# Optimization experiments

Hardware: AMD Instinct MI355X
Metric: run time of the kernel (lower is better)

The kernel has to match this reference:

```python
import jax, jax.numpy as jnp
import numpy as np
from jax.ops import segment_sum, segment_max

N_NODES = 50000
N_EDGES = 800000
N_GRAPHS = 512


def setup_inputs() -> dict:
    key = jax.random.key(0)
    ks = jax.random.split(key, 12)
    s = 0.1
    x = jax.random.normal(ks[0], (N_NODES, 3), dtype=jnp.float32)
    edge_index = jax.random.randint(ks[1], (2, N_EDGES), 0, N_NODES, dtype=jnp.int64)
    batch = jnp.sort(jax.random.randint(ks[2], (N_NODES,), 0, N_GRAPHS, dtype=jnp.int64))
    # GATConv(3, 64, heads=4): W [3, 4*64], att [4,64] each
    W1 = jax.random.normal(ks[3], (3, 256), dtype=jnp.float32) * s
    att_src1 = jax.random.normal(ks[4], (4, 64), dtype=jnp.float32) * s
    att_dst1 = jax.random.normal(ks[5], (4, 64), dtype=jnp.float32) * s
    bias1 = jnp.zeros((256,), dtype=jnp.float32)
    # GATConv(256, 128, heads=1)
    W2 = jax.random.normal(ks[6], (256, 128), dtype=jnp.float32) * s
    att_src2 = jax.random.normal(ks[7], (1, 128), dtype=jnp.float32) * s
    att_dst2 = jax.random.normal(ks[8], (1, 128), dtype=jnp.float32) * s
    bias2 = jnp.zeros((128,), dtype=jnp.float32)
    # Linear(128, 2)
    fcW = jax.random.normal(ks[9], (128, 2), dtype=jnp.float32) * s
    fcb = jnp.zeros((2,), dtype=jnp.float32)
    return {"x": x, "edge_index": edge_index, "batch": batch,
            "W1": W1, "att_src1": att_src1, "att_dst1": att_dst1, "bias1": bias1,
            "W2": W2, "att_src2": att_src2, "att_dst2": att_dst2, "bias2": bias2,
            "fcW": fcW, "fcb": fcb}


def gat_conv(x, src, dst, W, att_src, att_dst, bias):
    """PyG-style GATConv (concat heads). src->dst messages, softmax over dst."""
    N = x.shape[0]
    H, C = att_src.shape
    h = (x @ W).reshape(N, H, C)                      # [N,H,C]
    a_src = jnp.einsum('nhc,hc->nh', h, att_src)      # [N,H]
    a_dst = jnp.einsum('nhc,hc->nh', h, att_dst)      # [N,H]
    e = jax.nn.leaky_relu(a_src[src] + a_dst[dst], 0.2)  # [E,H]
    # segment softmax over incoming edges of each dst node
    emax = segment_max(e, dst, num_segments=N)        # [N,H]
    ee = jnp.exp(e - emax[dst])
    denom = segment_sum(ee, dst, num_segments=N)      # [N,H]
    alpha = ee / (denom[dst] + 1e-16)                 # [E,H]
    out = segment_sum(alpha[:, :, None] * h[src], dst, num_segments=N)  # [N,H,C]
    return out.reshape(N, H * C) + bias


def reference(x, edge_index, batch, W1, att_src1, att_dst1, bias1,
              W2, att_src2, att_dst2, bias2, fcW, fcb):
    N = x.shape[0]
    loops = jnp.arange(N, dtype=edge_index.dtype)
    src = jnp.concatenate([edge_index[0], loops])     # add self-loops (PyG default)
    dst = jnp.concatenate([edge_index[1], loops])
    h = jax.nn.relu(gat_conv(x, src, dst, W1, att_src1, att_dst1, bias1))
    h = jax.nn.relu(gat_conv(h, src, dst, W2, att_src2, att_dst2, bias2))
    # global mean pool per graph
    sums = segment_sum(h, batch, num_segments=N_GRAPHS)                # [G,128]
    counts = segment_sum(jnp.ones((N, 1), h.dtype), batch, num_segments=N_GRAPHS)
    pooled = sums / jnp.maximum(counts, 1.0)
    return pooled @ fcW + fcb                          # [G,2]
```

## Files before the change

### kernel.cpp

```cpp
#include <hip/hip_runtime.h>
#include <hip/hip_bf16.h>

#define NN 50000
#define NE 800000
#define ET (NN + NE)
#define NG 512
#define NCHUNK 196
#define NROWPAD 50048
#define CAP 64

#define NBUK 782
#define BCAP 1536
#define BSTRIDE 16

#define SCAT_BLKS 831
#define A1P_BLKS 196
#define W2B_BLKS 128
#define BND_BLKS 3
#define FRONT_GRID (SCAT_BLKS + A1P_BLKS + W2B_BLKS + BND_BLKS)

typedef __attribute__((ext_vector_type(8))) short bf16x8;
typedef __attribute__((ext_vector_type(4))) float f32x4;

static __device__ __forceinline__ float lrelu(float x) { return x > 0.f ? x : 0.2f * x; }

static __device__ __forceinline__ ushort f2b(float f) {
    __hip_bfloat16 b = __float2bfloat16(f);
    return *(ushort*)&b;
}
static __device__ __forceinline__ float b2f(ushort u) {
    union { unsigned int i; float f; } v; v.i = ((unsigned int)u) << 16; return v.f;
}

__global__ __launch_bounds__(256) void k_front(
        const int* __restrict__ ei, int* __restrict__ bcnt, unsigned int* __restrict__ bstore,
        const float* __restrict__ x, const float* __restrict__ W1,
        const float* __restrict__ attS1, const float* __restrict__ attD1,
        float* __restrict__ xa1, float* __restrict__ a1d,
        const float* __restrict__ W2, ushort* __restrict__ wtb,
        const int* __restrict__ batch, int* __restrict__ bounds) {
    __shared__ float wsd[24];
    int b = blockIdx.x, tid = threadIdx.x;
    if (b < SCAT_BLKS) {
        int t = b * 256 + tid;
        int base = t * 4;
        if (base >= ET) return;
        int4 sv, dv;
        if (base < NE) {
            sv = *(const int4*)(ei + base);
            dv = *(const int4*)(ei + NE + base);
        } else {
            int ls = base - NE;
            sv.x = ls; sv.y = ls + 1; sv.z = ls + 2; sv.w = ls + 3;
            dv = sv;
        }
        int b0 = dv.x >> 6, b1 = dv.y >> 6, b2 = dv.z >> 6, b3 = dv.w >> 6;
        int p0 = atomicAdd(&bcnt[b0 * BSTRIDE], 1);
        int p1 = atomicAdd(&bcnt[b1 * BSTRIDE], 1);
        int p2 = atomicAdd(&bcnt[b2 * BSTRIDE], 1);
        int p3 = atomicAdd(&bcnt[b3 * BSTRIDE], 1);
        bstore[b0 * BCAP + p0] = ((unsigned int)sv.x << 6) | (unsigned int)(dv.x & 63);
        bstore[b1 * BCAP + p1] = ((unsigned int)sv.y << 6) | (unsigned int)(dv.y & 63);
        bstore[b2 * BCAP + p2] = ((unsigned int)sv.z << 6) | (unsigned int)(dv.z & 63);
        bstore[b3 * BCAP + p3] = ((unsigned int)sv.w << 6) | (unsigned int)(dv.w & 63);
    } else if (b < SCAT_BLKS + A1P_BLKS) {
        if (tid < 24) {
            int sel = tid / 12, r = tid % 12;
            int i = r >> 2, h = r & 3;
            const float* att = sel ? attD1 : attS1;
            float s = 0.f;
            for (int c = 0; c < 64; c++) s += W1[i * 256 + h * 64 + c] * att[h * 64 + c];
            wsd[tid] = s;
        }
        __syncthreads();
        int n = (b - SCAT_BLKS) * 256 + tid;
        if (n >= NN) return;
        float x0 = x[n * 3], x1 = x[n * 3 + 1], x2 = x[n * 3 + 2];
        float4 r0, r1, dd;
        r0.x = x0; r0.y = x1; r0.z = x2;
        r0.w = x0 * wsd[0] + x1 * wsd[4] + x2 * wsd[8];
        r1.x = x0 * wsd[1] + x1 * wsd[5] + x2 * wsd[9];
        r1.y = x0 * wsd[2] + x1 * wsd[6] + x2 * wsd[10];
        r1.z = x0 * wsd[3] + x1 * wsd[7] + x2 * wsd[11];
        r1.w = 0.f;
        dd.x = x0 * wsd[12] + x1 * wsd[16] + x2 * wsd[20];
        dd.y = x0 * wsd[13] + x1 * wsd[17] + x2 * wsd[21];
        dd.z = x0 * wsd[14] + x1 * wsd[18] + x2 * wsd[22];
        dd.w = x0 * wsd[15] + x1 * wsd[19] + x2 * wsd[23];
        *(float4*)(xa1 + n * 8) = r0;
        *(float4*)(xa1 + n * 8 + 4) = r1;
        *(float4*)(a1d + n * 4) = dd;
    } else if (b < SCAT_BLKS + A1P_BLKS + W2B_BLKS) {
        int i = (b - SCAT_BLKS - A1P_BLKS) * 256 + tid;
        int k = i >> 7, c = i & 127;
        wtb[c * 256 + k] = f2b(W2[i]);
    } else {
        int g = (b - SCAT_BLKS - A1P_BLKS - W2B_BLKS) * 256 + tid;
        if (g > NG) return;
        int lo = 0, hi = NN;
        while (lo < hi) { int mid = (lo + hi) >> 1; if (batch[mid] < g) lo = mid + 1; else hi = mid; }
        bounds[g] = lo;
    }
}

__global__ __launch_bounds__(256) void k_csr(const int* __restrict__ bcnt,
                                             const unsigned int* __restrict__ bstore,
                                             ushort* __restrict__ csr, int* __restrict__ cnt) {
    __shared__ int cur[64];
    int b = blockIdx.x, tid = threadIdx.x;
    if (tid < 64) cur[tid] = 0;
    __syncthreads();
    int nb = bcnt[b * BSTRIDE];
    const unsigned int* bp = bstore + (size_t)b * BCAP;
    for (int i = tid; i < nb; i += 256) {
        unsigned int r = bp[i];
        int dlow = r & 63;
        int src = r >> 6;
        int pos = atomicAdd(&cur[dlow], 1);
        csr[(((size_t)b << 6) + dlow) * CAP + pos] = (ushort)src;
    }
    __syncthreads();
    if (tid < 64) {
        int node = (b << 6) + tid;
        if (node < NN) cnt[node] = cur[tid];
    }
}

__global__ void k_l1_aggr2(const float* __restrict__ xa1, const float* __restrict__ a1d,
                           const int* __restrict__ cnt, const ushort* __restrict__ csr,
                           float* __restrict__ xb) {
    int n = blockIdx.x * 256 + threadIdx.x;
    if (n >= NN) return;
    float4 ad = *(const float4*)(a1d + n * 4);
    int dg = cnt[n];
    const ushort* cp = csr + n * CAP;
    float a[4][3], l[4];
#pragma unroll
    for (int h = 0; h < 4; h++) { a[h][0] = a[h][1] = a[h][2] = 0.f; l[h] = 0.f; }
    int j = 0;
    for (; j + 4 <= dg; j += 4) {
        ushort4 ss = *(const ushort4*)(cp + j);
        int s0 = ss.x, s1 = ss.y, s2 = ss.z, s3 = ss.w;
        float4 p00 = *(const float4*)(xa1 + s0 * 8), p01 = *(const float4*)(xa1 + s0 * 8 + 4);
        float4 p10 = *(const float4*)(xa1 + s1 * 8), p11 = *(const float4*)(xa1 + s1 * 8 + 4);
        float4 p20 = *(const float4*)(xa1 + s2 * 8), p21 = *(const float4*)(xa1 + s2 * 8 + 4);
        float4 p30 = *(const float4*)(xa1 + s3 * 8), p31 = *(const float4*)(xa1 + s3 * 8 + 4);
#pragma unroll
        for (int q = 0; q < 4; q++) {
            float4 ra = (q == 0) ? p00 : (q == 1) ? p10 : (q == 2) ? p20 : p30;
            float4 rb = (q == 0) ? p01 : (q == 1) ? p11 : (q == 2) ? p21 : p31;
            float e0 = __expf(lrelu(ra.w + ad.x));
            float e1 = __expf(lrelu(rb.x + ad.y));
            float e2 = __expf(lrelu(rb.y + ad.z));
            float e3 = __expf(lrelu(rb.z + ad.w));
            a[0][0] = fmaf(e0, ra.x, a[0][0]); a[0][1] = fmaf(e0, ra.y, a[0][1]); a[0][2] = fmaf(e0, ra.z, a[0][2]); l[0] += e0;
            a[1][0] = fmaf(e1, ra.x, a[1][0]); a[1][1] = fmaf(e1, ra.y, a[1][1]); a[1][2] = fmaf(e1, ra.z, a[1][2]); l[1] += e1;
            a[2][0] = fmaf(e2, ra.x, a[2][0]); a[2][1] = fmaf(e2, ra.y, a[2][1]); a[2][2] = fmaf(e2, ra.z, a[2][2]); l[2] += e2;
            a[3][0] = fmaf(e3, ra.x, a[3][0]); a[3][1] = fmaf(e3, ra.y, a[3][1]); a[3][2] = fmaf(e3, ra.z, a[3][2]); l[3] += e3;
        }
    }
    for (; j < dg; j++) {
        int s = cp[j];
        float4 ra = *(const float4*)(xa1 + s * 8);
        float4 rb = *(const float4*)(xa1 + s * 8 + 4);
        float e0 = __expf(lrelu(ra.w + ad.x));
        float e1 = __expf(lrelu(rb.x + ad.y));
        float e2 = __expf(lrelu(rb.y + ad.z));
        float e3 = __expf(lrelu(rb.z + ad.w));
        a[0][0] = fmaf(e0, ra.x, a[0][0]); a[0][1] = fmaf(e0, ra.y, a[0][1]); a[0][2] = fmaf(e0, ra.z, a[0][2]); l[0] += e0;
        a[1][0] = fmaf(e1, ra.x, a[1][0]); a[1][1] = fmaf(e1, ra.y, a[1][1]); a[1][2] = fmaf(e1, ra.z, a[1][2]); l[1] += e1;
        a[2][0] = fmaf(e2, ra.x, a[2][0]); a[2][1] = fmaf(e2, ra.y, a[2][1]); a[2][2] = fmaf(e2, ra.z, a[2][2]); l[2] += e2;
        a[3][0] = fmaf(e3, ra.x, a[3][0]); a[3][1] = fmaf(e3, ra.y, a[3][1]); a[3][2] = fmaf(e3, ra.z, a[3][2]); l[3] += e3;
    }
    float o[12];
#pragma unroll
    for (int h = 0; h < 4; h++) {
        float inv = 1.f / (l[h] + 1e-16f);
        o[h * 3 + 0] = a[h][0] * inv;
        o[h * 3 + 1] = a[h][1] * inv;
        o[h * 3 + 2] = a[h][2] * inv;
    }
    *(float4*)(xb + n * 12) = *(float4*)(o);
    *(float4*)(xb + n * 12 + 4) = *(float4*)(o + 4);
    *(float4*)(xb + n * 12 + 8) = *(float4*)(o + 8);
}

__global__ __launch_bounds__(64) void k_gemm_mfma(
        const float* __restrict__ xb, const float* __restrict__ W1g,
        const float* __restrict__ b1g, const ushort* __restrict__ wtb,
        const float* __restrict__ attS2, const float* __restrict__ attD2,
        ushort* __restrict__ h2b, float* __restrict__ a2s, float* __restrict__ a2d) {
    __shared__ float W1s[768];
    __shared__ float b1s[256];
    int lane = threadIdx.x;
    int R = blockIdx.x * 32;
    if (R >= NN) return;
    for (int q = lane; q < 768; q += 64) W1s[q] = W1g[q];
    for (int q = lane; q < 256; q += 64) b1s[q] = b1g[q];
    __syncthreads();
    int row16 = lane & 15, kg = lane >> 4;

    float xr[2][12];
#pragma unroll
    for (int t = 0; t < 2; t++) {
        int row = R + t * 16 + row16;
        if (row < NN) {
            *(float4*)(&xr[t][0]) = *(const float4*)(xb + row * 12);
            *(float4*)(&xr[t][4]) = *(const float4*)(xb + row * 12 + 4);
            *(float4*)(&xr[t][8]) = *(const float4*)(xb + row * 12 + 8);
        } else {
#pragma unroll
            for (int q = 0; q < 12; q++) xr[t][q] = 0.f;
        }
    }

    f32x4 acc[2][8];
#pragma unroll
    for (int t = 0; t < 2; t++)
#pragma unroll
        for (int ct = 0; ct < 8; ct++) acc[t][ct] = (f32x4){0.f, 0.f, 0.f, 0.f};

    const ushort* Bb = wtb + (size_t)row16 * 256 + kg * 8;
#pragma unroll
    for (int s = 0; s < 8; s++) {
        int head = s >> 1;
        int c0 = s * 32 + kg * 8;
        bf16x8 a0, a1;
#pragma unroll
        for (int jj = 0; jj < 8; jj++) {
            int c = c0 + jj;
            float w0 = W1s[c], w1 = W1s[256 + c], w2 = W1s[512 + c], bb = b1s[c];
            float v0 = fmaxf(fmaf(xr[0][head * 3], w0, fmaf(xr[0][head * 3 + 1], w1, fmaf(xr[0][head * 3 + 2], w2, bb))), 0.f);
            float v1 = fmaxf(fmaf(xr[1][head * 3], w0, fmaf(xr[1][head * 3 + 1], w1, fmaf(xr[1][head * 3 + 2], w2, bb))), 0.f);
            a0[jj] = (short)f2b(v0);
            a1[jj] = (short)f2b(v1);
        }
#pragma unroll
        for (int ct = 0; ct < 8; ct++) {
            bf16x8 bfr = *(const bf16x8*)(Bb + ct * 16 * 256 + s * 32);
            acc[0][ct] = __builtin_amdgcn_mfma_f32_16x16x32_bf16(a0, bfr, acc[0][ct], 0, 0, 0);
            acc[1][ct] = __builtin_amdgcn_mfma_f32_16x16x32_bf16(a1, bfr, acc[1][ct], 0, 0, 0);
        }
    }

    float s2v[8], d2v[8];
#pragma unroll
    for (int ct = 0; ct < 8; ct++) {
        s2v[ct] = attS2[ct * 16 + row16];
        d2v[ct] = attD2[ct * 16 + row16];
    }
#pragma unroll
    for (int tau = 0; tau < 2; tau++) {
#pragma unroll
        for (int q = 0; q < 4; q++) {
            int row = R + tau * 16 + kg * 4 + q;
            float ps = 0.f, pd = 0.f;
            if (row < NN) {
#pragma unroll
                for (int ct = 0; ct < 8; ct++) {
                    float v = acc[tau][ct][q];
                    h2b[(size_t)row * 128 + ct * 16 + row16] = f2b(v);
                    ps = fmaf(v, s2v[ct], ps);
                    pd = fmaf(v, d2v[ct], pd);
                }
            }
            for (int o = 1; o < 16; o <<= 1) {
                ps += __shfl_xor(ps, o, 64);
                pd += __shfl_xor(pd, o, 64);
            }
            if (row < NN && row16 == 0) { a2s[row] = ps; a2d[row] = pd; }
        }
    }
}

__global__ void k_l2_aggr(const ushort* __restrict__ h2u, const float* __restrict__ a2s,
                          const float* __restrict__ a2d, const int* __restrict__ cnt,
                          const ushort* __restrict__ csr, const float* __restrict__ b2,
                          float* __restrict__ out2) {
    int n = blockIdx.x, t = threadIdx.x;
    float adm = a2d[n];
    int dg = cnt[n];
    const ushort* cp = csr + n * CAP;
    float accx = 0.f, accy = 0.f, l = 0.f;
    int j = 0;
    for (; j + 8 <= dg; j += 8) {
        ushort4 sA = *(const ushort4*)(cp + j);
        ushort4 sB = *(const ushort4*)(cp + j + 4);
        int s0 = sA.x, s1 = sA.y, s2 = sA.z, s3 = sA.w;
        int s4 = sB.x, s5 = sB.y, s6 = sB.z, s7 = sB.w;
        float e0 = a2s[s0], e1 = a2s[s1], e2 = a2s[s2], e3 = a2s[s3];
        float e4 = a2s[s4], e5 = a2s[s5], e6 = a2s[s6], e7 = a2s[s7];
        ushort2 u0 = *(const ushort2*)(h2u + (size_t)s0 * 128 + t * 2);
        ushort2 u1 = *(const ushort2*)(h2u + (size_t)s1 * 128 + t * 2);
        ushort2 u2 = *(const ushort2*)(h2u + (size_t)s2 * 128 + t * 2);
        ushort2 u3 = *(const ushort2*)(h2u + (size_t)s3 * 128 + t * 2);
        ushort2 u4 = *(const ushort2*)(h2u + (size_t)s4 * 128 + t * 2);
        ushort2 u5 = *(const ushort2*)(h2u + (size_t)s5 * 128 + t * 2);
        ushort2 u6 = *(const ushort2*)(h2u + (size_t)s6 * 128 + t * 2);
        ushort2 u7 = *(const ushort2*)(h2u + (size_t)s7 * 128 + t * 2);
        float p0 = __expf(lrelu(e0 + adm)), p1 = __expf(lrelu(e1 + adm));
        float p2 = __expf(lrelu(e2 + adm)), p3 = __expf(lrelu(e3 + adm));
        float p4 = __expf(lrelu(e4 + adm)), p5 = __expf(lrelu(e5 + adm));
        float p6 = __expf(lrelu(e6 + adm)), p7 = __expf(lrelu(e7 + adm));
        accx = fmaf(p0, b2f(u0.x), fmaf(p1, b2f(u1.x), fmaf(p2, b2f(u2.x), fmaf(p3, b2f(u3.x), accx))));
        accx = fmaf(p4, b2f(u4.x), fmaf(p5, b2f(u5.x), fmaf(p6, b2f(u6.x), fmaf(p7, b2f(u7.x), accx))));
        accy = fmaf(p0, b2f(u0.y), fmaf(p1, b2f(u1.y), fmaf(p2, b2f(u2.y), fmaf(p3, b2f(u3.y), accy))));
        accy = fmaf(p4, b2f(u4.y), fmaf(p5, b2f(u5.y), fmaf(p6, b2f(u6.y), fmaf(p7, b2f(u7.y), accy))));
        l += (p0 + p1) + (p2 + p3) + (p4 + p5) + (p6 + p7);
    }
    for (; j < dg; j++) {
        int s = cp[j];
        float p = __expf(lrelu(a2s[s] + adm));
        ushort2 u = *(const ushort2*)(h2u + (size_t)s * 128 + t * 2);
        accx = fmaf(p, b2f(u.x), accx);
        accy = fmaf(p, b2f(u.y), accy);
        l += p;
    }
    float inv = 1.f / (l + 1e-16f);
    int c = t * 2;
    float2 o;
    o.x = fmaxf(accx * inv + b2[c], 0.f);
    o.y = fmaxf(accy * inv + b2[c + 1], 0.f);
    *(float2*)(out2 + n * 128 + c) = o;
}

__global__ void k_pool_fc(const float* __restrict__ out2, const int* __restrict__ bounds,
                          const float* __restrict__ fcW, const float* __restrict__ fcb,
                          float* __restrict__ out) {
    int g = blockIdx.x, t = threadIdx.x;
    int s = bounds[g], e = bounds[g + 1];
    float s0 = 0.f, s1 = 0.f, s2 = 0.f, s3 = 0.f;
    int n = s;
    for (; n + 4 <= e; n += 4) {
        s0 += out2[n * 128 + t];
        s1 += out2[(n + 1) * 128 + t];
        s2 += out2[(n + 2) * 128 + t];
        s3 += out2[(n + 3) * 128 + t];
    }
    for (; n < e; n++) s0 += out2[n * 128 + t];
    float sum = (s0 + s1) + (s2 + s3);
    float cnt = (float)(e - s);
    float pooled = sum / fmaxf(cnt, 1.f);
    float p0 = pooled * fcW[t * 2 + 0];
    float p1 = pooled * fcW[t * 2 + 1];
    for (int o = 32; o; o >>= 1) {
        p0 += __shfl_down(p0, o, 64);
        p1 += __shfl_down(p1, o, 64);
    }
    __shared__ float l0[2], l1[2];
    if ((t & 63) == 0) { l0[t >> 6] = p0; l1[t >> 6] = p1; }
    __syncthreads();
    if (t == 0) {
        out[g * 2 + 0] = l0[0] + l0[1] + fcb[0];
        out[g * 2 + 1] = l1[0] + l1[1] + fcb[1];
    }
}

extern "C" void kernel_launch(void* const* d_in, const int* in_sizes, int n_in,
                              void* d_out, int out_size, void* d_ws, size_t ws_size,
                              hipStream_t stream) {
    (void)in_sizes; (void)n_in; (void)out_size; (void)ws_size;
    const float* x     = (const float*)d_in[0];
    const int*   ei    = (const int*)d_in[1];
    const int*   batch = (const int*)d_in[2];
    const float* W1    = (const float*)d_in[3];
    const float* attS1 = (const float*)d_in[4];
    const float* attD1 = (const float*)d_in[5];
    const float* b1    = (const float*)d_in[6];
    const float* W2    = (const float*)d_in[7];
    const float* attS2 = (const float*)d_in[8];
    const float* attD2 = (const float*)d_in[9];
    const float* b2    = (const float*)d_in[10];
    const float* fcW   = (const float*)d_in[11];
    const float* fcb   = (const float*)d_in[12];
    float* out = (float*)d_out;

    char* ws = (char*)d_ws;
    size_t off = 0;
    auto alloc = [&](size_t bytes) -> char* {
        char* p = ws + off;
        off = (off + bytes + 255) & ~(size_t)255;
        return p;
    };
    float*  xa1  = (float*)alloc((size_t)NN * 8 * 4);
    float*  a1d  = (float*)alloc((size_t)NN * 4 * 4);
    float*  xb   = (float*)alloc((size_t)NN * 12 * 4);
    int*    cnt  = (int*)alloc((size_t)NN * 4);
    ushort* csr  = (ushort*)alloc((size_t)NN * CAP * 2);
    int*    bcnt = (int*)alloc((size_t)NBUK * BSTRIDE * 4);
    unsigned int* bstore = (unsigned int*)alloc((size_t)NBUK * BCAP * 4);
    ushort* wtb  = (ushort*)alloc((size_t)128 * 256 * 2);
    ushort* h2b  = (ushort*)alloc((size_t)NN * 128 * 2);
    float*  a2s  = (float*)alloc((size_t)NN * 4);
    float*  a2d  = (float*)alloc((size_t)NN * 4);
    int*    bounds = (int*)alloc((size_t)(NG + 1) * 4);
    float*  out2 = (float*)alloc((size_t)NN * 128 * 4);

    hipMemsetAsync(bcnt, 0, (size_t)NBUK * BSTRIDE * 4, stream);
    k_front<<<FRONT_GRID, 256, 0, stream>>>(ei, bcnt, bstore, x, W1, attS1, attD1,
                                            xa1, a1d, W2, wtb, batch, bounds);
    k_csr<<<NBUK, 256, 0, stream>>>(bcnt, bstore, csr, cnt);
    k_l1_aggr2<<<NCHUNK, 256, 0, stream>>>(xa1, a1d, cnt, csr, xb);
    k_gemm_mfma<<<(NROWPAD / 32), 64, 0, stream>>>(xb, W1, b1, wtb, attS2, attD2, h2b, a2s, a2d);
    k_l2_aggr<<<NN, 64, 0, stream>>>(h2b, a2s, a2d, cnt, csr, b2, out2);
    k_pool_fc<<<NG, 128, 0, stream>>>(out2, bounds, fcW, fcb, out);
}
```

Before: 154.9 us.

## Pre-bin edges in shared memory before global bucket scatter, add self-loops in CSR

Each scatter block now bins its 1024 edges by destination into shared-memory sub-buckets of 256 nodes, then reserves space in the global bucket with one atomic per bin and writes the records out contiguously. This replaces per-edge global atomics on 782 buckets with far fewer atomics on 196 larger buckets. Self-loops are no longer scattered as edges; the CSR kernel appends them directly per node. The risks are overflow of the fixed 32-slot local bins and 5120-slot global buckets, plus the shared-memory footprint of roughly 26KB per block, which may limit occupancy.

```diff
diff --git a/kernel.cpp b/kernel.cpp
--- a/kernel.cpp
+++ b/kernel.cpp
@@ -3,17 +3,17 @@
 
 #define NN 50000
 #define NE 800000
-#define ET (NN + NE)
 #define NG 512
 #define NCHUNK 196
 #define NROWPAD 50048
 #define CAP 64
 
-#define NBUK 782
-#define BCAP 1536
+#define NBUK 196
+#define BCAP 5120
 #define BSTRIDE 16
-
-#define SCAT_BLKS 831
+#define LBCAP 32
+
+#define SCAT_BLKS 782
 #define A1P_BLKS 196
 #define W2B_BLKS 128
 #define BND_BLKS 3
@@ -39,31 +39,43 @@
         float* __restrict__ xa1, float* __restrict__ a1d,
         const float* __restrict__ W2, ushort* __restrict__ wtb,
         const int* __restrict__ batch, int* __restrict__ bounds) {
-    __shared__ float wsd[24];
     int b = blockIdx.x, tid = threadIdx.x;
     if (b < SCAT_BLKS) {
+        __shared__ unsigned int lrec[NBUK * LBCAP];
+        __shared__ int lcnt[NBUK];
+        __shared__ int lbase[NBUK];
+        for (int i = tid; i < NBUK; i += 256) lcnt[i] = 0;
+        __syncthreads();
         int t = b * 256 + tid;
-        int base = t * 4;
-        if (base >= ET) return;
-        int4 sv, dv;
-        if (base < NE) {
-            sv = *(const int4*)(ei + base);
-            dv = *(const int4*)(ei + NE + base);
-        } else {
-            int ls = base - NE;
-            sv.x = ls; sv.y = ls + 1; sv.z = ls + 2; sv.w = ls + 3;
-            dv = sv;
-        }
-        int b0 = dv.x >> 6, b1 = dv.y >> 6, b2 = dv.z >> 6, b3 = dv.w >> 6;
-        int p0 = atomicAdd(&bcnt[b0 * BSTRIDE], 1);
-        int p1 = atomicAdd(&bcnt[b1 * BSTRIDE], 1);
-        int p2 = atomicAdd(&bcnt[b2 * BSTRIDE], 1);
-        int p3 = atomicAdd(&bcnt[b3 * BSTRIDE], 1);
-        bstore[b0 * BCAP + p0] = ((unsigned int)sv.x << 6) | (unsigned int)(dv.x & 63);
-        bstore[b1 * BCAP + p1] = ((unsigned int)sv.y << 6) | (unsigned int)(dv.y & 63);
-        bstore[b2 * BCAP + p2] = ((unsigned int)sv.z << 6) | (unsigned int)(dv.z & 63);
-        bstore[b3 * BCAP + p3] = ((unsigned int)sv.w << 6) | (unsigned int)(dv.w & 63);
+        int base4 = t * 4;
+        if (base4 < NE) {
+            int4 sv = *(const int4*)(ei + base4);
+            int4 dv = *(const int4*)(ei + NE + base4);
+            int d, s, bin, p;
+            d = dv.x; s = sv.x; bin = d >> 8;
+            p = atomicAdd(&lcnt[bin], 1);
+            lrec[bin * LBCAP + p] = ((unsigned int)s << 8) | (unsigned int)(d & 255);
+            d = dv.y; s = sv.y; bin = d >> 8;
+            p = atomicAdd(&lcnt[bin], 1);
+            lrec[bin * LBCAP + p] = ((unsigned int)s << 8) | (unsigned int)(d & 255);
+            d = dv.z; s = sv.z; bin = d >> 8;
+            p = atomicAdd(&lcnt[bin], 1);
+            lrec[bin * LBCAP + p] = ((unsigned int)s << 8) | (unsigned int)(d & 255);
+            d = dv.w; s = sv.w; bin = d >> 8;
+            p = atomicAdd(&lcnt[bin], 1);
+            lrec[bin * LBCAP + p] = ((unsigned int)s << 8) | (unsigned int)(d & 255);
+        }
+        __syncthreads();
+        for (int i = tid; i < NBUK; i += 256)
+            lbase[i] = lcnt[i] ? atomicAdd(&bcnt[i * BSTRIDE], lcnt[i]) : 0;
+        __syncthreads();
+        for (int i = tid; i < NBUK * LBCAP; i += 256) {
+            int bin = i >> 5, pos = i & (LBCAP - 1);
+            if (pos < lcnt[bin])
+                bstore[(size_t)bin * BCAP + lbase[bin] + pos] = lrec[i];
+        }
     } else if (b < SCAT_BLKS + A1P_BLKS) {
+        __shared__ float wsd[24];
         if (tid < 24) {
             int sel = tid / 12, r = tid % 12;
             int i = r >> 2, h = r & 3;
@@ -106,23 +118,25 @@
 __global__ __launch_bounds__(256) void k_csr(const int* __restrict__ bcnt,
                                              const unsigned int* __restrict__ bstore,
                                              ushort* __restrict__ csr, int* __restrict__ cnt) {
-    __shared__ int cur[64];
+    __shared__ int cur[256];
     int b = blockIdx.x, tid = threadIdx.x;
-    if (tid < 64) cur[tid] = 0;
+    cur[tid] = 0;
     __syncthreads();
     int nb = bcnt[b * BSTRIDE];
     const unsigned int* bp = bstore + (size_t)b * BCAP;
     for (int i = tid; i < nb; i += 256) {
         unsigned int r = bp[i];
-        int dlow = r & 63;
-        int src = r >> 6;
+        int dlow = r & 255;
+        int src = r >> 8;
         int pos = atomicAdd(&cur[dlow], 1);
-        csr[(((size_t)b << 6) + dlow) * CAP + pos] = (ushort)src;
+        csr[(((size_t)b << 8) + dlow) * CAP + pos] = (ushort)src;
     }
     __syncthreads();
-    if (tid < 64) {
-        int node = (b << 6) + tid;
-        if (node < NN) cnt[node] = cur[tid];
+    int node = (b << 8) + tid;
+    if (node < NN) {
+        int c = cur[tid];
+        csr[(size_t)node * CAP + c] = (ushort)node;
+        cnt[node] = c + 1;
     }
 }
 
@@ -133,7 +147,7 @@
     if (n >= NN) return;
     float4 ad = *(const float4*)(a1d + n * 4);
     int dg = cnt[n];
-    const ushort* cp = csr + n * CAP;
+    const ushort* cp = csr + (size_t)n * CAP;
     float a[4][3], l[4];
 #pragma unroll
     for (int h = 0; h < 4; h++) { a[h][0] = a[h][1] = a[h][2] = 0.f; l[h] = 0.f; }
@@ -280,7 +294,7 @@
     int n = blockIdx.x, t = threadIdx.x;
     float adm = a2d[n];
     int dg = cnt[n];
-    const ushort* cp = csr + n * CAP;
+    const ushort* cp = csr + (size_t)n * CAP;
     float accx = 0.f, accy = 0.f, l = 0.f;
     int j = 0;
     for (; j + 8 <= dg; j += 8) {
```

Measured after the change: 125.6 us. 18.9% less time.
